# Kernel optimization log

Hardware: AMD Instinct MI355X
Metric: run time of the kernel (lower is better)

## Reference

```python
import jax, jax.numpy as jnp
import numpy as np

NBIT = 8
NSPLIT = 255.0  # 2**NBIT - 1


def _quantized_matmul(x, w_clean, eps):
    # Faithful port of quantization(): bit-slice x into NBIT binary planes, run a
    # noisy linear per plane with weight w + randn*|w|*0.1, and sum. The 8
    # sequential fc() calls are fused into one einsum over the bit axis.
    # x: (..., in); w_clean: (out, in); eps: (NBIT, out, in) standard normal.
    mn = jnp.min(x)
    mx = jnp.max(x)
    q = ((x - mn) / (mx - mn) * NSPLIT).astype(jnp.uint8).astype(jnp.int32)  # truncating cast as in torch
    quant_base = 2 ** jnp.arange(NBIT, dtype=jnp.int32)
    binary = ((q[..., None] & quant_base) != 0).astype(x.dtype)              # (..., in, NBIT)
    scaled = binary * (2.0 ** jnp.arange(NBIT)).astype(x.dtype)              # plane i scaled by 2**i
    w_noisy = w_clean[None] + eps * jnp.abs(w_clean)[None] * 0.1             # (NBIT, out, in)
    z = jnp.einsum('...ib,boi->...o', scaled, w_noisy)
    return z, mn, mx, w_noisy[-1]  # fc.weight after loop == last noisy weight


def _forward(node_embedding, edge_embedding, nbr_mask, cond1, cond2, eps1, eps2, bn_gamma, bn_beta):
    B, At, Nbr, Fe = edge_embedding.shape
    Fn = node_embedding.shape[-1]
    c1 = jnp.concatenate(
        [jnp.broadcast_to(node_embedding[:, :, None, :], (B, At, Nbr, Fn)), edge_embedding],
        axis=3)                                                              # (B, At, Nbr, Fn+Fe)
    # quantization + re_quantization through fc (re-quant uses last noisy fc.weight)
    z1, mn1, mx1, w_last = _quantized_matmul(c1, cond1[0], eps1)
    bias1 = jnp.sum(mn1 * w_last, axis=1)                                    # (H1,)
    h = jax.nn.relu(z1 / NSPLIT * (mx1 - mn1) + bias1)                       # (B, At, Nbr, H1)
    # quantization + re_quantization through fc_2 (re-quant uses conductance[1][-1])
    z2, mn2, mx2, _ = _quantized_matmul(h, cond2[0], eps2)
    bias2 = jnp.sum(mn2 * cond2[-1], axis=1)                                 # (2*Fn,)
    c2 = z2 / NSPLIT * (mx2 - mn2) + bias2                                   # (B, At, Nbr, 2*Fn)
    nbr_gate, nbr_extract = jnp.split(c2, 2, axis=3)
    nbr_sumed = jax.nn.sigmoid(nbr_gate) * jnp.tanh(nbr_extract) * nbr_mask[..., None]
    nbr_sumed = jnp.sum(nbr_sumed, axis=2)                                   # (B, At, Fn)
    # BatchNorm1d in training mode: batch statistics over flattened (B*At)
    flat = nbr_sumed.reshape(-1, Fn)
    mean = jnp.mean(flat, axis=0)
    var = jnp.var(flat, axis=0)  # biased variance, as torch BN uses for normalization
    bn = ((flat - mean) / jnp.sqrt(var + 1e-5) * bn_gamma + bn_beta).reshape(B, At, Fn)
    return jax.nn.relu(node_embedding + bn)


def setup_inputs() -> dict:
    key = jax.random.key(0)
    ks = jax.random.split(key, 7)
    B, At, Nbr, Fn, Fe = 16, 96, 12, 64, 64
    H1, H2 = 4 * (Fn + Fe), 2 * Fn
    return {
        'node_embedding': jax.random.normal(ks[0], (B, At, Fn), jnp.float32),
        'edge_embedding': jax.random.normal(ks[1], (B, At, Nbr, Fe), jnp.float32),
        'nbr_mask': (jax.random.uniform(ks[2], (B, At, Nbr)) > 0.5).astype(jnp.float32),
        'cond1': jax.random.normal(ks[3], (2, H1, Fn + Fe), jnp.float32) * 0.05,
        'cond2': jax.random.normal(ks[4], (2, H2, H1), jnp.float32) * 0.05,
        'eps1': jax.random.normal(ks[5], (NBIT, H1, Fn + Fe), jnp.float32),
        'eps2': jax.random.normal(ks[6], (NBIT, H2, H1), jnp.float32),
        'bn_gamma': jnp.ones((Fn,), jnp.float32),
        'bn_beta': jnp.zeros((Fn,), jnp.float32),
    }


def reference(node_embedding, edge_embedding, nbr_mask, cond1, cond2, eps1, eps2, bn_gamma, bn_beta):
    return _forward(node_embedding, edge_embedding, nbr_mask, cond1, cond2, eps1, eps2, bn_gamma, bn_beta)
```

## Files before the change

### kernel.cpp

```cpp
#include <hip/hip_runtime.h>
#include <stdint.h>

#define B_    16
#define AT_   96
#define NBR_  12
#define FN_   64
#define FE_   64
#define M1    (B_*AT_*NBR_)
#define R_    (B_*AT_)
#define K1Q   128
#define N1    512
#define K2Q   512
#define N2    128
#define SPLIT2 4

typedef _Float16 f16x8 __attribute__((ext_vector_type(8)));
typedef float    f32x4 __attribute__((ext_vector_type(4)));
typedef __attribute__((address_space(1))) const void gconst_void;
typedef __attribute__((address_space(3))) void lds_void;

#define OFF_SCAL  0u
#define OFF_B1R   256u
#define OFF_B2R   (OFF_B1R + 2048u)
#define OFF_Q1    4096u
#define OFF_W1E   (OFF_Q1  + (size_t)M1*K1Q)
#define OFF_W2E   (OFF_W1E + (size_t)N1*K1Q*8*2)
#define OFF_Q2    (OFF_W2E + (size_t)N2*K2Q*8*2)
#define OFF_H     (OFF_Q2  + (size_t)M1*K2Q)
#define OFF_ZP    OFF_H
#define OFF_NS    (OFF_H   + (size_t)M1*N1*4)

__device__ __forceinline__ unsigned int enc_f(float f) {
    unsigned int u = __float_as_uint(f);
    return (u & 0x80000000u) ? ~u : (u | 0x80000000u);
}
__device__ __forceinline__ float dec_f(unsigned int u) {
    return __uint_as_float((u & 0x80000000u) ? (u & 0x7FFFFFFFu) : ~u);
}

__global__ void k_init(unsigned int* scal, float* b1raw, float* b2raw) {
    int t = threadIdx.x;
    if (t == 0) { scal[0] = 0xFFFFFFFFu; scal[1] = 0u; scal[2] = 0xFFFFFFFFu; scal[3] = 0u; }
    if (t < N1) b1raw[t] = 0.f;
    if (t < N2) b2raw[t] = 0.f;
}

__global__ __launch_bounds__(256) void k_minmax_c1(const float* __restrict__ node,
                                                   const float* __restrict__ edge,
                                                   unsigned int* __restrict__ scal) {
    const int nn = B_*AT_*FN_;
    const int ntot = nn + M1*FE_;
    float mn = 3.0e38f, mx = -3.0e38f;
    for (int idx = blockIdx.x*blockDim.x + threadIdx.x; idx < ntot; idx += gridDim.x*blockDim.x) {
        float x = (idx < nn) ? node[idx] : edge[idx - nn];
        mn = fminf(mn, x); mx = fmaxf(mx, x);
    }
    __shared__ float smn[256], smx[256];
    smn[threadIdx.x] = mn; smx[threadIdx.x] = mx; __syncthreads();
    for (int s = 128; s > 0; s >>= 1) {
        if (threadIdx.x < s) {
            smn[threadIdx.x] = fminf(smn[threadIdx.x], smn[threadIdx.x+s]);
            smx[threadIdx.x] = fmaxf(smx[threadIdx.x], smx[threadIdx.x+s]);
        }
        __syncthreads();
    }
    if (threadIdx.x == 0) { atomicMin(&scal[0], enc_f(smn[0])); atomicMax(&scal[1], enc_f(smx[0])); }
}

template<int KQ, int N, int SBASE, bool USE_SECOND>
__global__ __launch_bounds__(256) void k_prep_w16(const float* __restrict__ w_clean,
                                                  const float* __restrict__ eps,
                                                  const unsigned int* __restrict__ scal,
                                                  float* __restrict__ braw,
                                                  _Float16* __restrict__ We) {
    int idx = blockIdx.x*blockDim.x + threadIdx.x;
    if (idx >= N*KQ) return;
    int o = idx / KQ;
    int i = idx % KQ;
    float mn = dec_f(scal[SBASE]), mx = dec_f(scal[SBASE+1]);
    float s = (mx - mn) * (1.0f/255.0f);
    float w = w_clean[idx];
    float aw = fabsf(w) * 0.1f;
    union { _Float16 h[8]; uint4 u; } pk;
    float p = s;
    float v7 = 0.f;
    #pragma unroll
    for (int b = 0; b < 8; b++) {
        float e = eps[(size_t)b*N*KQ + idx];
        float v = w + e*aw;
        if (b == 7) v7 = v;
        pk.h[b] = (_Float16)(v * p);
        p *= 2.0f;
    }
    *(uint4*)&We[((size_t)o*KQ + i)*8] = pk.u;
    float bv = USE_SECOND ? w_clean[(size_t)N*KQ + idx] : v7;
    #pragma unroll
    for (int off = 32; off > 0; off >>= 1) bv += __shfl_down(bv, off);
    if ((threadIdx.x & 63) == 0) atomicAdd(&braw[o], bv);
}

__global__ __launch_bounds__(256) void k_quant_c1(const float* __restrict__ node,
                                                  const float* __restrict__ edge,
                                                  const unsigned int* __restrict__ scal,
                                                  unsigned int* __restrict__ q1) {
    int idx = blockIdx.x*256 + threadIdx.x;
    int m = idx >> 5, dw = idx & 31;
    const float mn = dec_f(scal[0]), rng = dec_f(scal[1]) - mn;
    float4 x;
    if (dw < 16) x = *(const float4*)&node[(m/NBR_)*FN_ + dw*4];
    else         x = *(const float4*)&edge[(size_t)m*FE_ + (dw-16)*4];
    unsigned int b0 = (unsigned char)(int)((x.x - mn) / rng * 255.0f);
    unsigned int b1 = (unsigned char)(int)((x.y - mn) / rng * 255.0f);
    unsigned int b2 = (unsigned char)(int)((x.z - mn) / rng * 255.0f);
    unsigned int b3 = (unsigned char)(int)((x.w - mn) / rng * 255.0f);
    q1[idx] = b0 | (b1 << 8) | (b2 << 16) | (b3 << 24);
}

__global__ __launch_bounds__(256) void k_quant_h(const float* __restrict__ h,
                                                 const unsigned int* __restrict__ scal,
                                                 unsigned int* __restrict__ q2) {
    int idx = blockIdx.x*256 + threadIdx.x;
    const float mn = dec_f(scal[2]), rng = dec_f(scal[3]) - mn;
    float4 x = *(const float4*)&h[(size_t)idx*4];
    unsigned int b0 = (unsigned char)(int)((x.x - mn) / rng * 255.0f);
    unsigned int b1 = (unsigned char)(int)((x.y - mn) / rng * 255.0f);
    unsigned int b2 = (unsigned char)(int)((x.z - mn) / rng * 255.0f);
    unsigned int b3 = (unsigned char)(int)((x.w - mn) / rng * 255.0f);
    q2[idx] = b0 | (b1 << 8) | (b2 << 16) | (b3 << 24);
}

__device__ __forceinline__ f16x8 expand_byte(unsigned int byte) {
    unsigned int r2 = byte | (byte << 15);
    union { unsigned int u[4]; f16x8 h; } t;
    t.u[0] = ( r2       & 0x00010001u) * 0x3C00u;
    t.u[1] = ((r2 >> 2) & 0x00010001u) * 0x3C00u;
    t.u[2] = ((r2 >> 4) & 0x00010001u) * 0x3C00u;
    t.u[3] = ((r2 >> 6) & 0x00010001u) * 0x3C00u;
    return t.h;
}

template<int KQ, int N, int SPLITK, bool EPI1>
__global__ __launch_bounds__(256, 4) void kg(const unsigned char* __restrict__ q,
                                             const _Float16* __restrict__ W,
                                             const float* __restrict__ braw,
                                             void* __restrict__ outv,
                                             unsigned int* __restrict__ scal) {
    constexpr int KP  = KQ * 8;
    constexpr int KPS = KP / SPLITK;
    constexpr int NIT = KPS / 128;
    __shared__ _Float16 Bs[16384];
    __shared__ uint2    Qs[512];

    const int tid  = threadIdx.x;
    const int lane = tid & 63;
    const int w    = tid >> 6;
    const int wm   = (w & 1) * 64;
    const int kg   = w >> 1;
    const int l15  = lane & 15;
    const int lq   = lane >> 4;
    const int sh8  = lq * 8;
    const int m0   = blockIdx.x * 128;
    const int o0   = blockIdx.y * 64;
    const int kbase = blockIdx.z * KPS;

    f32x4 acc[4][4] = {};

    unsigned int bo[4];
    #pragma unroll
    for (int iss = 0; iss < 4; ++iss) {
        int s = iss*256 + tid, skg = s >> 9, sg = s & 511, n = sg >> 3;
        int csrc = (sg & 7) ^ (n & 7);
        bo[iss] = (unsigned int)((o0 + n)*KP + kbase + skg*512 + csrc*8);
    }
    const int bdl = (tid & ~63) * 8;

    unsigned int ao[2];
    #pragma unroll
    for (int i = 0; i < 2; ++i) {
        int d = w*128 + i*64 + lane;
        int kga = d >> 8, row = (d >> 1) & 127, half = d & 1;
        ao[i] = (unsigned int)((m0 + row)*KQ + (kbase >> 3) + kga*64 + half*4);
    }
    const int adl = w * 512;

    auto stage = [&](int IT, int BUF) {
        #pragma unroll
        for (int iss = 0; iss < 4; ++iss)
            __builtin_amdgcn_global_load_lds((gconst_void*)(W + bo[iss] + IT*64),
                (lds_void*)(Bs + BUF*8192 + iss*2048 + bdl), 16, 0, 0);
        #pragma unroll
        for (int i = 0; i < 2; ++i)
            __builtin_amdgcn_global_load_lds((gconst_void*)(q + ao[i] + IT*8),
                (lds_void*)((char*)Qs + BUF*2048 + i*256 + adl), 4, 0, 0);
    };

    auto compute = [&](int cur) {
        const _Float16* Bc = Bs + cur*8192 + kg*4096;
        const uint2*    Qc = Qs + cur*256 + kg*128;
        uint2 qd[4];
        #pragma unroll
        for (int mf = 0; mf < 4; ++mf)
            qd[mf] = Qc[wm + mf*16 + l15];
        #pragma unroll
        for (int kf = 0; kf < 2; ++kf) {
            f16x8 bf[4];
            #pragma unroll
            for (int nf = 0; nf < 4; ++nf) {
                const int nl = nf*16 + l15;
                const int ch = kf*4 + lq;
                bf[nf] = *(const f16x8*)&Bc[nl*64 + ((ch ^ (nl & 7)) << 3)];
            }
            #pragma unroll
            for (int mf = 0; mf < 4; ++mf) {
                unsigned int byte = ((kf ? qd[mf].y : qd[mf].x) >> sh8) & 0xFFu;
                f16x8 a = expand_byte(byte);
                #pragma unroll
                for (int nf = 0; nf < 4; ++nf)
                    acc[mf][nf] = __builtin_amdgcn_mfma_f32_16x16x32_f16(a, bf[nf], acc[mf][nf], 0, 0, 0);
            }
        }
    };

    stage(0, 0);
    #pragma unroll 1
    for (int it = 0; it < NIT-1; ++it) {
        const int cur = it & 1;
        stage(it+1, cur ^ 1);
        asm volatile("s_waitcnt vmcnt(6)" ::: "memory");
        asm volatile("s_barrier" ::: "memory");
        compute(cur);
        asm volatile("s_waitcnt lgkmcnt(0)" ::: "memory");
        asm volatile("s_barrier" ::: "memory");
    }
    asm volatile("s_waitcnt vmcnt(0)" ::: "memory");
    asm volatile("s_barrier" ::: "memory");
    compute((NIT-1) & 1);

    float* red = (float*)Bs;
    #pragma unroll
    for (int nf = 0; nf < 4; ++nf) {
        __syncthreads();
        if (kg == 1) {
            #pragma unroll
            for (int mf = 0; mf < 4; ++mf)
                *(f32x4*)&red[(w & 1)*1024 + mf*256 + lane*4] = acc[mf][nf];
        }
        __syncthreads();
        if (kg == 0) {
            #pragma unroll
            for (int mf = 0; mf < 4; ++mf)
                acc[mf][nf] += *(const f32x4*)&red[(w & 1)*1024 + mf*256 + lane*4];
        }
    }

    if (EPI1) {
        float tmn = 3.0e38f, tmx = -3.0e38f;
        if (kg == 0) {
            float* out = (float*)outv;
            const float mn1 = dec_f(scal[0]);
            float bv[4];
            #pragma unroll
            for (int nf = 0; nf < 4; ++nf) bv[nf] = mn1 * braw[o0 + nf*16 + l15];
            #pragma unroll
            for (int mf = 0; mf < 4; ++mf) {
                const int mr = m0 + wm + mf*16 + lq*4;
                #pragma unroll
                for (int nf = 0; nf < 4; ++nf) {
                    const int oc = o0 + nf*16 + l15;
                    #pragma unroll
                    for (int r = 0; r < 4; ++r) {
                        float v = acc[mf][nf][r] + bv[nf];
                        v = fmaxf(v, 0.0f);
                        tmn = fminf(tmn, v); tmx = fmaxf(tmx, v);
                        out[(size_t)(mr + r)*N + oc] = v;
                    }
                }
            }
        }
        __syncthreads();
        red[tid] = tmn; red[256 + tid] = tmx;
        __syncthreads();
        for (int s = 128; s > 0; s >>= 1) {
            if (tid < s) {
                red[tid]       = fminf(red[tid],       red[tid + s]);
                red[256 + tid] = fmaxf(red[256 + tid], red[256 + tid + s]);
            }
            __syncthreads();
        }
        if (tid == 0) { atomicMin(&scal[2], enc_f(red[0])); atomicMax(&scal[3], enc_f(red[256])); }
    } else {
        if (kg == 0) {
            _Float16* op = (_Float16*)outv + (size_t)blockIdx.z * ((size_t)M1 * N);
            #pragma unroll
            for (int mf = 0; mf < 4; ++mf) {
                const int mr = m0 + wm + mf*16 + lq*4;
                #pragma unroll
                for (int nf = 0; nf < 4; ++nf) {
                    const int oc = o0 + nf*16 + l15;
                    #pragma unroll
                    for (int r = 0; r < 4; ++r)
                        op[(size_t)(mr + r)*N + oc] = (_Float16)acc[mf][nf][r];
                }
            }
        }
    }
}

__global__ __launch_bounds__(256) void k_nbr(const _Float16* __restrict__ zp,
                                             const float* __restrict__ b2raw,
                                             const unsigned int* __restrict__ scal,
                                             const float* __restrict__ mask,
                                             float* __restrict__ ns) {
    const size_t SP = (size_t)M1 * N2;
    int tid = threadIdx.x;
    int r = blockIdx.x*4 + (tid >> 6);
    int f = tid & 63;
    const float mn2 = dec_f(scal[2]);
    float bg = mn2 * b2raw[f], be = mn2 * b2raw[64 + f];
    float s = 0.f;
    #pragma unroll
    for (int n = 0; n < NBR_; n++) {
        int m = r*NBR_ + n;
        size_t base = (size_t)m * N2;
        float g = bg, e = be;
        #pragma unroll
        for (int z = 0; z < SPLIT2; z++) {
            g += (float)zp[z*SP + base + f];
            e += (float)zp[z*SP + base + 64 + f];
        }
        float sig = 1.0f / (1.0f + expf(-g));
        s += sig * tanhf(e) * mask[m];
    }
    ns[r*64 + f] = s;
}

__global__ __launch_bounds__(256) void k_bn(const float* __restrict__ ns,
                                            const float* __restrict__ node,
                                            const float* __restrict__ gamma,
                                            const float* __restrict__ beta,
                                            float* __restrict__ out) {
    int f = blockIdx.x;
    int tid = threadIdx.x;
    float x[6];
    float s = 0.f, ss = 0.f;
    #pragma unroll
    for (int k = 0; k < 6; k++) {
        int r = tid + k*256;
        x[k] = ns[r*64 + f];
        s += x[k]; ss += x[k]*x[k];
    }
    __shared__ float rs[256], rss[256];
    rs[tid] = s; rss[tid] = ss; __syncthreads();
    for (int st = 128; st > 0; st >>= 1) {
        if (tid < st) { rs[tid] += rs[tid+st]; rss[tid] += rss[tid+st]; }
        __syncthreads();
    }
    float mean = rs[0] / 1536.0f;
    float var  = rss[0] / 1536.0f - mean*mean;
    float denom = sqrtf(var + 1e-5f);
    float g = gamma[f], bt = beta[f];
    #pragma unroll
    for (int k = 0; k < 6; k++) {
        int r = tid + k*256;
        float v = node[r*64 + f] + ((x[k] - mean) / denom * g + bt);
        out[r*64 + f] = fmaxf(v, 0.f);
    }
}

extern "C" void kernel_launch(void* const* d_in, const int* in_sizes, int n_in,
                              void* d_out, int out_size, void* d_ws, size_t ws_size,
                              hipStream_t stream) {
    const float* node  = (const float*)d_in[0];
    const float* edge  = (const float*)d_in[1];
    const float* mask  = (const float*)d_in[2];
    const float* cond1 = (const float*)d_in[3];
    const float* cond2 = (const float*)d_in[4];
    const float* eps1  = (const float*)d_in[5];
    const float* eps2  = (const float*)d_in[6];
    const float* gamma = (const float*)d_in[7];
    const float* beta  = (const float*)d_in[8];
    float* out = (float*)d_out;
    char* ws = (char*)d_ws;

    unsigned int*  scal = (unsigned int*)(ws + OFF_SCAL);
    float* b1raw = (float*)(ws + OFF_B1R);
    float* b2raw = (float*)(ws + OFF_B2R);
    unsigned char* q1 = (unsigned char*)(ws + OFF_Q1);
    _Float16* W1e = (_Float16*)(ws + OFF_W1E);
    _Float16* W2e = (_Float16*)(ws + OFF_W2E);
    unsigned char* q2 = (unsigned char*)(ws + OFF_Q2);
    float*    h  = (float*)(ws + OFF_H);
    _Float16* zp = (_Float16*)(ws + OFF_ZP);
    float*    ns = (float*)(ws + OFF_NS);

    k_init<<<1, 1024, 0, stream>>>(scal, b1raw, b2raw);
    k_minmax_c1<<<512, 256, 0, stream>>>(node, edge, scal);
    k_prep_w16<K1Q, N1, 0, false><<<(N1*K1Q + 255)/256, 256, 0, stream>>>(cond1, eps1, scal, b1raw, W1e);
    k_quant_c1<<<(M1*32)/256, 256, 0, stream>>>(node, edge, scal, (unsigned int*)q1);
    kg<K1Q, N1, 1, true><<<dim3(M1/128, N1/64, 1), 256, 0, stream>>>(q1, W1e, b1raw, h, scal);
    k_prep_w16<K2Q, N2, 2, true><<<(N2*K2Q + 255)/256, 256, 0, stream>>>(cond2, eps2, scal, b2raw, W2e);
    k_quant_h<<<(M1*128)/256, 256, 0, stream>>>(h, scal, (unsigned int*)q2);
    kg<K2Q, N2, SPLIT2, false><<<dim3(M1/128, N2/64, SPLIT2), 256, 0, stream>>>(q2, W2e, b2raw, zp, scal);
    k_nbr<<<R_/4, 256, 0, stream>>>(zp, b2raw, scal, mask, ns);
    k_bn<<<64, 256, 0, stream>>>(ns, node, gamma, beta, out);
}
```

Measured before the change: 201.4 us.

## Pre-tile quantized activations so GEMM loads whole A tile upfront

The quant kernels now write the byte-quantized activations in a block-tiled, k-chunk-major layout through an LDS transpose. The GEMM then loads its entire A slice (16 KB) into LDS once with wide 16-byte async loads, instead of streaming 4-byte loads per iteration alongside B. MFMA sections are also wrapped in s_setprio to favour the math wave. This removes many small A loads from the inner pipeline. In exchange it adds LDS use that may lower occupancy and puts an extra shared-memory pass into the quant kernels.

```diff
diff --git a/kernel.cpp b/kernel.cpp
--- a/kernel.cpp
+++ b/kernel.cpp
@@ -76,7 +76,6 @@
     int idx = blockIdx.x*blockDim.x + threadIdx.x;
     if (idx >= N*KQ) return;
     int o = idx / KQ;
-    int i = idx % KQ;
     float mn = dec_f(scal[SBASE]), mx = dec_f(scal[SBASE+1]);
     float s = (mx - mn) * (1.0f/255.0f);
     float w = w_clean[idx];
@@ -92,7 +91,7 @@
         pk.h[b] = (_Float16)(v * p);
         p *= 2.0f;
     }
-    *(uint4*)&We[((size_t)o*KQ + i)*8] = pk.u;
+    *(uint4*)&We[(size_t)idx*8] = pk.u;
     float bv = USE_SECOND ? w_clean[(size_t)N*KQ + idx] : v7;
     #pragma unroll
     for (int off = 32; off > 0; off >>= 1) bv += __shfl_down(bv, off);
@@ -102,31 +101,54 @@
 __global__ __launch_bounds__(256) void k_quant_c1(const float* __restrict__ node,
                                                   const float* __restrict__ edge,
                                                   const unsigned int* __restrict__ scal,
-                                                  unsigned int* __restrict__ q1) {
-    int idx = blockIdx.x*256 + threadIdx.x;
-    int m = idx >> 5, dw = idx & 31;
+                                                  unsigned int* __restrict__ qt) {
+    __shared__ unsigned int T[128*33];
+    const int mblk = blockIdx.x, t = threadIdx.x;
     const float mn = dec_f(scal[0]), rng = dec_f(scal[1]) - mn;
-    float4 x;
-    if (dw < 16) x = *(const float4*)&node[(m/NBR_)*FN_ + dw*4];
-    else         x = *(const float4*)&edge[(size_t)m*FE_ + (dw-16)*4];
-    unsigned int b0 = (unsigned char)(int)((x.x - mn) / rng * 255.0f);
-    unsigned int b1 = (unsigned char)(int)((x.y - mn) / rng * 255.0f);
-    unsigned int b2 = (unsigned char)(int)((x.z - mn) / rng * 255.0f);
-    unsigned int b3 = (unsigned char)(int)((x.w - mn) / rng * 255.0f);
-    q1[idx] = b0 | (b1 << 8) | (b2 << 16) | (b3 << 24);
+    #pragma unroll
+    for (int r = 0; r < 16; ++r) {
+        int p = r*256 + t;
+        int row = p >> 5, c4 = p & 31, j = c4*4;
+        int m = mblk*128 + row;
+        float4 x = (j < 64) ? *(const float4*)&node[(m/NBR_)*FN_ + j]
+                            : *(const float4*)&edge[(size_t)m*FE_ + (j-64)];
+        unsigned int b0 = (unsigned char)(int)((x.x - mn) / rng * 255.0f);
+        unsigned int b1 = (unsigned char)(int)((x.y - mn) / rng * 255.0f);
+        unsigned int b2 = (unsigned char)(int)((x.z - mn) / rng * 255.0f);
+        unsigned int b3 = (unsigned char)(int)((x.w - mn) / rng * 255.0f);
+        T[row*33 + c4] = b0 | (b1 << 8) | (b2 << 16) | (b3 << 24);
+    }
+    __syncthreads();
+    #pragma unroll
+    for (int r = 0; r < 16; ++r) {
+        int o = r*256 + t;
+        qt[(size_t)mblk*4096 + o] = T[(t>>1)*33 + r*2 + (t&1)];
+    }
 }
 
 __global__ __launch_bounds__(256) void k_quant_h(const float* __restrict__ h,
                                                  const unsigned int* __restrict__ scal,
-                                                 unsigned int* __restrict__ q2) {
-    int idx = blockIdx.x*256 + threadIdx.x;
+                                                 unsigned int* __restrict__ qt) {
+    __shared__ unsigned int T[128*33];
+    const int mblk = blockIdx.x, jc = blockIdx.y, t = threadIdx.x;
     const float mn = dec_f(scal[2]), rng = dec_f(scal[3]) - mn;
-    float4 x = *(const float4*)&h[(size_t)idx*4];
-    unsigned int b0 = (unsigned char)(int)((x.x - mn) / rng * 255.0f);
-    unsigned int b1 = (unsigned char)(int)((x.y - mn) / rng * 255.0f);
-    unsigned int b2 = (unsigned char)(int)((x.z - mn) / rng * 255.0f);
-    unsigned int b3 = (unsigned char)(int)((x.w - mn) / rng * 255.0f);
-    q2[idx] = b0 | (b1 << 8) | (b2 << 16) | (b3 << 24);
+    #pragma unroll
+    for (int r = 0; r < 16; ++r) {
+        int p = r*256 + t;
+        int row = p >> 5, c4 = p & 31;
+        float4 x = *(const float4*)&h[(size_t)(mblk*128 + row)*512 + jc*128 + c4*4];
+        unsigned int b0 = (unsigned char)(int)((x.x - mn) / rng * 255.0f);
+        unsigned int b1 = (unsigned char)(int)((x.y - mn) / rng * 255.0f);
+        unsigned int b2 = (unsigned char)(int)((x.z - mn) / rng * 255.0f);
+        unsigned int b3 = (unsigned char)(int)((x.w - mn) / rng * 255.0f);
+        T[row*33 + c4] = b0 | (b1 << 8) | (b2 << 16) | (b3 << 24);
+    }
+    __syncthreads();
+    #pragma unroll
+    for (int r = 0; r < 16; ++r) {
+        int o = r*256 + t;
+        qt[(size_t)mblk*16384 + (size_t)jc*4096 + o] = T[(t>>1)*33 + r*2 + (t&1)];
+    }
 }
 
 __device__ __forceinline__ f16x8 expand_byte(unsigned int byte) {
@@ -149,7 +171,7 @@
     constexpr int KPS = KP / SPLITK;
     constexpr int NIT = KPS / 128;
     __shared__ _Float16 Bs[16384];
-    __shared__ uint2    Qs[512];
+    __shared__ __align__(16) unsigned char As[16384];
 
     const int tid  = threadIdx.x;
     const int lane = tid & 63;
@@ -174,33 +196,26 @@
     }
     const int bdl = (tid & ~63) * 8;
 
-    unsigned int ao[2];
-    #pragma unroll
-    for (int i = 0; i < 2; ++i) {
-        int d = w*128 + i*64 + lane;
-        int kga = d >> 8, row = (d >> 1) & 127, half = d & 1;
-        ao[i] = (unsigned int)((m0 + row)*KQ + (kbase >> 3) + kga*64 + half*4);
-    }
-    const int adl = w * 512;
-
-    auto stage = [&](int IT, int BUF) {
+    const unsigned char* aq = q + (size_t)blockIdx.x*((size_t)KQ*128) + (size_t)blockIdx.z*16384;
+    #pragma unroll
+    for (int r = 0; r < 4; ++r)
+        __builtin_amdgcn_global_load_lds((gconst_void*)(aq + r*4096 + tid*16),
+            (lds_void*)(As + r*4096 + (tid & ~63)*16), 16, 0, 0);
+
+    auto stageB = [&](int IT, int BUF) {
         #pragma unroll
         for (int iss = 0; iss < 4; ++iss)
             __builtin_amdgcn_global_load_lds((gconst_void*)(W + bo[iss] + IT*64),
                 (lds_void*)(Bs + BUF*8192 + iss*2048 + bdl), 16, 0, 0);
-        #pragma unroll
-        for (int i = 0; i < 2; ++i)
-            __builtin_amdgcn_global_load_lds((gconst_void*)(q + ao[i] + IT*8),
-                (lds_void*)((char*)Qs + BUF*2048 + i*256 + adl), 4, 0, 0);
     };
 
-    auto compute = [&](int cur) {
+    auto compute = [&](int cur, int it) {
         const _Float16* Bc = Bs + cur*8192 + kg*4096;
-        const uint2*    Qc = Qs + cur*256 + kg*128;
+        const unsigned char* Ac = As + kg*8192 + it*1024;
         uint2 qd[4];
         #pragma unroll
         for (int mf = 0; mf < 4; ++mf)
-            qd[mf] = Qc[wm + mf*16 + l15];
+            qd[mf] = *(const uint2*)&Ac[(wm + mf*16 + l15)*8];
         #pragma unroll
         for (int kf = 0; kf < 2; ++kf) {
             f16x8 bf[4];
@@ -210,6 +225,7 @@
                 const int ch = kf*4 + lq;
                 bf[nf] = *(const f16x8*)&Bc[nl*64 + ((ch ^ (nl & 7)) << 3)];
             }
+            __builtin_amdgcn_s_setprio(1);
             #pragma unroll
             for (int mf = 0; mf < 4; ++mf) {
                 unsigned int byte = ((kf ? qd[mf].y : qd[mf].x) >> sh8) & 0xFFu;
@@ -218,23 +234,24 @@
                 for (int nf = 0; nf < 4; ++nf)
                     acc[mf][nf] = __builtin_amdgcn_mfma_f32_16x16x32_f16(a, bf[nf], acc[mf][nf], 0, 0, 0);
             }
+            __builtin_amdgcn_s_setprio(0);
         }
     };
 
-    stage(0, 0);
+    stageB(0, 0);
     #pragma unroll 1
     for (int it = 0; it < NIT-1; ++it) {
         const int cur = it & 1;
-        stage(it+1, cur ^ 1);
-        asm volatile("s_waitcnt vmcnt(6)" ::: "memory");
+        stageB(it+1, cur ^ 1);
+        asm volatile("s_waitcnt vmcnt(4)" ::: "memory");
         asm volatile("s_barrier" ::: "memory");
-        compute(cur);
+        compute(cur, it);
         asm volatile("s_waitcnt lgkmcnt(0)" ::: "memory");
         asm volatile("s_barrier" ::: "memory");
     }
     asm volatile("s_waitcnt vmcnt(0)" ::: "memory");
     asm volatile("s_barrier" ::: "memory");
-    compute((NIT-1) & 1);
+    compute((NIT-1) & 1, NIT-1);
 
     float* red = (float*)Bs;
     #pragma unroll
@@ -396,10 +413,10 @@
     k_init<<<1, 1024, 0, stream>>>(scal, b1raw, b2raw);
     k_minmax_c1<<<512, 256, 0, stream>>>(node, edge, scal);
     k_prep_w16<K1Q, N1, 0, false><<<(N1*K1Q + 255)/256, 256, 0, stream>>>(cond1, eps1, scal, b1raw, W1e);
-    k_quant_c1<<<(M1*32)/256, 256, 0, stream>>>(node, edge, scal, (unsigned int*)q1);
+    k_quant_c1<<<M1/128, 256, 0, stream>>>(node, edge, scal, (unsigned int*)q1);
     kg<K1Q, N1, 1, true><<<dim3(M1/128, N1/64, 1), 256, 0, stream>>>(q1, W1e, b1raw, h, scal);
     k_prep_w16<K2Q, N2, 2, true><<<(N2*K2Q + 255)/256, 256, 0, stream>>>(cond2, eps2, scal, b2raw, W2e);
-    k_quant_h<<<(M1*128)/256, 256, 0, stream>>>(h, scal, (unsigned int*)q2);
+    k_quant_h<<<dim3(M1/128, 4), 256, 0, stream>>>(h, scal, (unsigned int*)q2);
     kg<K2Q, N2, SPLIT2, false><<<dim3(M1/128, N2/64, SPLIT2), 256, 0, stream>>>(q2, W2e, b2raw, zp, scal);
     k_nbr<<<R_/4, 256, 0, stream>>>(zp, b2raw, scal, mask, ns);
     k_bn<<<64, 256, 0, stream>>>(ns, node, gamma, beta, out);
```

Result: slower. 218.5 us (+8.5%).
